# Kernel tuning notes

Hardware: AMD Instinct MI355X
Metric: run time of the kernel (lower is better)

The kernel has to match this reference:

```python
import jax, jax.numpy as jnp
import numpy as np

BETA = 0.25  # commit loss weight (init arg beta)


def setup_inputs() -> dict:
    key = jax.random.key(0)
    k1, k2 = jax.random.split(key)
    z = jax.random.normal(k1, (8, 8192, 128), dtype=jnp.float32)          # (B, T, D)
    codebook = jax.random.normal(k2, (1024, 128), dtype=jnp.float32)      # (K, D)
    return {"z": z, "codebook": codebook}


def reference(z, codebook):
    # distances: ||z - e||^2 = -2 z.e + ||z||^2 + ||e||^2
    dot = jnp.einsum('btd,kd->btk', z, codebook)                 # (B, T, K)
    norm_sq_z = jnp.sum(jnp.square(z), axis=-1, keepdims=True)   # (B, T, 1)
    norm_sq_e = jnp.sum(jnp.square(codebook), axis=-1)           # (K,)
    dist = -2.0 * dot + norm_sq_z + norm_sq_e                    # (B, T, K)
    ids = jnp.argmin(dist, axis=-1)                              # (B, T) int
    z_q = codebook[ids]                                          # gather -> (B, T, D)
    similarity = dot / jnp.sqrt(norm_sq_z) / jnp.sqrt(norm_sq_e) # cosine sim (B, T, K)
    # VQ loss (mean over batch*time of L2 norms along channel axis)
    loss_codebook = jnp.mean(jnp.linalg.norm(z - jax.lax.stop_gradient(z_q), axis=-1))
    loss_commit = jnp.mean(jnp.linalg.norm(jax.lax.stop_gradient(z) - z_q, axis=-1))
    loss_vq = loss_codebook + BETA * loss_commit
    return z_q, similarity, ids, loss_vq
```

## Files before the change

kernel.cpp:

```cpp
#include <hip/hip_runtime.h>
#include <hip/hip_bf16.h>


#define BT_TOTAL 65536
#define DDIM 128
#define KCODES 1024
#define ROWS 64
#define KC 64
#define NCHUNK (KCODES / KC)
#define TAU 0.125f


__global__ __launch_bounds__(256) void vq_pre_transpose(const float* __restrict__ e,
                                                        float* __restrict__ e_t) {
    int g = blockIdx.x * 256 + threadIdx.x;
    int d = g >> 10;
    int k = g & 1023;
    e_t[d * KCODES + k] = e[k * DDIM + d];
}

__global__ __launch_bounds__(256) void vq_pre_norms(const float* __restrict__ e,
                                                    float* __restrict__ ne,
                                                    float* __restrict__ ine) {
    int code = blockIdx.x * 4 + (threadIdx.x >> 6);
    int lane = threadIdx.x & 63;
    float v0 = e[code * DDIM + lane];
    float v1 = e[code * DDIM + lane + 64];
    float s = v0 * v0 + v1 * v1;
    #pragma unroll
    for (int m = 1; m < 64; m <<= 1) s += __shfl_xor(s, m);
    if (lane == 0) { ne[code] = s; ine[code] = rsqrtf(s); }
}


__global__ __launch_bounds__(256, 2) void vq_main(
    const float* __restrict__ z, const float* __restrict__ cb,
    const float* __restrict__ e_t, const float* __restrict__ ne_g,
    const float* __restrict__ ine_g,
    float* __restrict__ zq_out, float* __restrict__ sim_out,
    float* __restrict__ ids_out, float* __restrict__ loss_out,
    int* __restrict__ fix_cnt, int* __restrict__ fix_rows)
{
    __shared__ float lds_z[DDIM][ROWS];
    __shared__ float lds_e[DDIM][KC];
    __shared__ float lds_nzp[4][ROWS];
    __shared__ float lds_nz[ROWS];
    __shared__ float lds_inz[ROWS];
    __shared__ int   lds_best[ROWS];
    __shared__ float lds_loss[16];

    const int t = threadIdx.x;
    const int row_base = blockIdx.x * ROWS;

    #pragma unroll
    for (int it = 0; it < 8; ++it) {
        int idx = t + 256 * it;
        int row = idx & 63;
        int q   = idx >> 6;
        const float4 v = reinterpret_cast<const float4*>(z)[(size_t)(row_base + row) * 32 + q];
        lds_z[4 * q + 0][row] = v.x;
        lds_z[4 * q + 1][row] = v.y;
        lds_z[4 * q + 2][row] = v.z;
        lds_z[4 * q + 3][row] = v.w;
    }
    __syncthreads();

    {
        int row = t & 63, dp = t >> 6;
        float s = 0.f;
        #pragma unroll 8
        for (int d0 = 0; d0 < 32; ++d0) {
            float v = lds_z[dp * 32 + d0][row];
            s = fmaf(v, v, s);
        }
        lds_nzp[dp][row] = s;
    }
    __syncthreads();
    if (t < ROWS) {
        float s = lds_nzp[0][t] + lds_nzp[1][t] + lds_nzp[2][t] + lds_nzp[3][t];
        lds_nz[t]  = s;
        lds_inz[t] = rsqrtf(s);
    }
    __syncthreads();

    const int r = t >> 4;
    const int c = t & 15;

    float nzr[4], inzr[4];
    #pragma unroll
    for (int i = 0; i < 4; ++i) { nzr[i] = lds_nz[4 * r + i]; inzr[i] = lds_inz[4 * r + i]; }

    float runmin[4], runmin2[4]; int runidx[4];
    #pragma unroll
    for (int i = 0; i < 4; ++i) { runmin[i] = 3.4e38f; runmin2[i] = 3.4e38f; runidx[i] = 0; }

    for (int chunk = 0; chunk < NCHUNK; ++chunk) {
        const int kb = chunk * KC;

        #pragma unroll
        for (int j = 0; j < 8; ++j) {
            int idx = t + 256 * j;
            int d  = idx >> 4;
            int cc = idx & 15;
            float4 v = reinterpret_cast<const float4*>(e_t)[d * (KCODES / 4) + (kb >> 2) + cc];
            *reinterpret_cast<float4*>(&lds_e[d][4 * cc]) = v;
        }
        __syncthreads();

        float acc[4][4];
        #pragma unroll
        for (int i = 0; i < 4; ++i)
            #pragma unroll
            for (int j = 0; j < 4; ++j) acc[i][j] = 0.f;

        #pragma unroll 8
        for (int d = 0; d < DDIM; ++d) {
            float4 zv = *reinterpret_cast<const float4*>(&lds_z[d][4 * r]);
            float4 ev = *reinterpret_cast<const float4*>(&lds_e[d][4 * c]);
            float za[4] = { zv.x, zv.y, zv.z, zv.w };
            float ea[4] = { ev.x, ev.y, ev.z, ev.w };
            #pragma unroll
            for (int i = 0; i < 4; ++i)
                #pragma unroll
                for (int j = 0; j < 4; ++j)
                    acc[i][j] = fmaf(za[i], ea[j], acc[i][j]);
        }

        const float4 nev  = reinterpret_cast<const float4*>(ne_g)[chunk * 16 + c];
        const float4 inev = reinterpret_cast<const float4*>(ine_g)[chunk * 16 + c];
        float nea[4]  = { nev.x, nev.y, nev.z, nev.w };
        float inea[4] = { inev.x, inev.y, inev.z, inev.w };

        #pragma unroll
        for (int i = 0; i < 4; ++i) {
            float sa[4];
            #pragma unroll
            for (int j = 0; j < 4; ++j) {
                float dot = acc[i][j];
                sa[j] = dot * inzr[i] * inea[j];
                float dd = ((-2.0f * dot) + nzr[i]) + nea[j];
                int kidx = kb + 4 * c + j;
                if (dd < runmin[i]) { runmin2[i] = runmin[i]; runmin[i] = dd; runidx[i] = kidx; }
                else if (dd < runmin2[i]) runmin2[i] = dd;
            }
            float4 sv; sv.x = sa[0]; sv.y = sa[1]; sv.z = sa[2]; sv.w = sa[3];
            reinterpret_cast<float4*>(sim_out)[(size_t)(row_base + 4 * r + i) * (KCODES / 4) + (kb >> 2) + c] = sv;
        }
        __syncthreads();
    }

    #pragma unroll
    for (int m = 1; m < 16; m <<= 1) {
        #pragma unroll
        for (int i = 0; i < 4; ++i) {
            float om1 = __shfl_xor(runmin[i], m);
            float om2 = __shfl_xor(runmin2[i], m);
            int   oi  = __shfl_xor(runidx[i], m);
            float nm2 = fminf(fminf(runmin2[i], om2), fmaxf(runmin[i], om1));
            if (om1 < runmin[i] || (om1 == runmin[i] && oi < runidx[i])) {
                runmin[i] = om1; runidx[i] = oi;
            }
            runmin2[i] = nm2;
        }
    }
    if (c == 0) {
        float psum = 0.f;
        #pragma unroll
        for (int i = 0; i < 4; ++i) {
            int row = 4 * r + i;
            lds_best[row] = runidx[i];
            ids_out[row_base + row] = (float)runidx[i];
            psum += sqrtf(fmaxf(runmin[i], 0.f));
            if (runmin2[i] - runmin[i] < TAU) {
                int slot = atomicAdd(fix_cnt, 1);
                fix_rows[slot] = row_base + row;
            }
        }
        lds_loss[r] = psum;
    }
    __syncthreads();

    if (t == 0) {
        float s = 0.f;
        #pragma unroll
        for (int i = 0; i < 16; ++i) s += lds_loss[i];
        atomicAdd(loss_out, s * (1.25f / 65536.0f));
    }

    #pragma unroll
    for (int j2 = 0; j2 < 8; ++j2) {
        int idx = t + 256 * j2;
        int row = idx >> 5;
        int q   = idx & 31;
        int b   = lds_best[row];
        float4 v = reinterpret_cast<const float4*>(cb)[b * 32 + q];
        reinterpret_cast<float4*>(zq_out)[(size_t)(row_base + row) * 32 + q] = v;
    }
}


__global__ __launch_bounds__(256) void vq_fixup(
    const float* __restrict__ z, const float* __restrict__ cb,
    const float* __restrict__ e_t,
    const int* __restrict__ fix_cnt, const int* __restrict__ fix_rows,
    float* __restrict__ zq_out, float* __restrict__ ids_out)
{
    __shared__ float zl[DDIM];
    __shared__ double wbest[4];
    __shared__ int    wbidx[4];
    const int n = *fix_cnt;
    const int tid = threadIdx.x;

    for (int item = blockIdx.x; item < n; item += gridDim.x) {
        const int row = fix_rows[item];
        if (tid < DDIM) zl[tid] = z[(size_t)row * DDIM + tid];
        __syncthreads();

        double bd = 1.0e300; int bi = 0;
        #pragma unroll
        for (int c4 = 0; c4 < 4; ++c4) {
            const int code = c4 * 256 + tid;
            double acc = 0.0;
            #pragma unroll 4
            for (int d = 0; d < DDIM; ++d) {
                double diff = (double)zl[d] - (double)e_t[d * KCODES + code];
                acc = fma(diff, diff, acc);
            }
            if (acc < bd) { bd = acc; bi = code; }
        }
        const int lane = tid & 63, w = tid >> 6;
        #pragma unroll
        for (int m = 1; m < 64; m <<= 1) {
            double od = __shfl_xor(bd, m);
            int    oi = __shfl_xor(bi, m);
            if (od < bd || (od == bd && oi < bi)) { bd = od; bi = oi; }
        }
        if (lane == 0) { wbest[w] = bd; wbidx[w] = bi; }
        __syncthreads();
        if (tid == 0) {
            double b0 = wbest[0]; int i0 = wbidx[0];
            #pragma unroll
            for (int i = 1; i < 4; ++i)
                if (wbest[i] < b0 || (wbest[i] == b0 && wbidx[i] < i0)) { b0 = wbest[i]; i0 = wbidx[i]; }
            wbidx[0] = i0;
            ids_out[row] = (float)i0;
        }
        __syncthreads();
        const int b = wbidx[0];
        if (tid < 32) {
            float4 v = reinterpret_cast<const float4*>(cb)[b * 32 + tid];
            reinterpret_cast<float4*>(zq_out)[(size_t)row * 32 + tid] = v;
        }
        __syncthreads();
    }
}


extern "C" void kernel_launch(void* const* d_in, const int* in_sizes, int n_in,
                              void* d_out, int out_size, void* d_ws, size_t ws_size,
                              hipStream_t stream) {
    const float* z  = (const float*)d_in[0];
    const float* cb = (const float*)d_in[1];

    float* out  = (float*)d_out;
    float* zq   = out;
    float* sim  = out + 8388608;
    float* ids  = out + 75497472;
    float* loss = out + 75563008;

    float* e_t      = (float*)d_ws;
    float* ne       = e_t + 131072;
    float* ine      = ne + 1024;
    int*   fix_cnt  = (int*)(ine + 1024);
    int*   fix_rows = fix_cnt + 1;

    hipMemsetAsync(loss, 0, sizeof(float), stream);
    hipMemsetAsync(fix_cnt, 0, sizeof(int), stream);

    vq_pre_transpose<<<512, 256, 0, stream>>>(cb, e_t);
    vq_pre_norms<<<256, 256, 0, stream>>>(cb, ne, ine);
    vq_main<<<BT_TOTAL / ROWS, 256, 0, stream>>>(z, cb, e_t, ne, ine,
                                                 zq, sim, ids, loss, fix_cnt, fix_rows);
    vq_fixup<<<256, 256, 0, stream>>>(z, cb, e_t, fix_cnt, fix_rows, zq, ids);
}
```

Baseline: 690.8 us.

## Compute distance GEMM with split-bf16 MFMA instead of FP32 FMA

Replaces the LDS-tiled FP32 FMA dot-product loop with bf16 MFMA instructions, using a hi/lo bf16 split of both z and the codebook and three MFMAs to approximate FP32 precision. Each wave keeps its 32 rows of z in registers and streams codebook fragments directly from global memory without LDS staging. Row norms of z now come from a separate pre-pass kernel, and the codebook is pre-split into bf16 hi/lo arrays. The risks are reduced dot-product precision that the tau-based fixup has to absorb, and a similarity store pattern of scalar, strided writes that may coalesce worse than the earlier float4 stores.

```diff
diff --git a/kernel.cpp b/kernel.cpp
--- a/kernel.cpp
+++ b/kernel.cpp
@@ -5,18 +5,38 @@
 #define BT_TOTAL 65536
 #define DDIM 128
 #define KCODES 1024
-#define ROWS 64
-#define KC 64
-#define NCHUNK (KCODES / KC)
 #define TAU 0.125f
 
-
-__global__ __launch_bounds__(256) void vq_pre_transpose(const float* __restrict__ e,
-                                                        float* __restrict__ e_t) {
-    int g = blockIdx.x * 256 + threadIdx.x;
-    int d = g >> 10;
-    int k = g & 1023;
-    e_t[d * KCODES + k] = e[k * DDIM + d];
+typedef __attribute__((ext_vector_type(8))) short bf16x8;
+typedef __attribute__((ext_vector_type(4))) float f32x4;
+
+__device__ __forceinline__ unsigned short f32_to_bf16_rne(float x) {
+    unsigned int u = __float_as_uint(x);
+    unsigned int r = u + 0x7FFFu + ((u >> 16) & 1u);
+    return (unsigned short)(r >> 16);
+}
+__device__ __forceinline__ float bf16u_to_f32(unsigned short s) {
+    return __uint_as_float(((unsigned int)s) << 16);
+}
+
+
+__global__ __launch_bounds__(256) void vq_pre_cb(const float* __restrict__ cb,
+                                                 unsigned short* __restrict__ cb_hi,
+                                                 unsigned short* __restrict__ cb_lo) {
+    int gidx = blockIdx.x * 256 + threadIdx.x;
+    float4 v = reinterpret_cast<const float4*>(cb)[gidx];
+    float a[4] = { v.x, v.y, v.z, v.w };
+    ushort4 h, l;
+    unsigned short hs[4], ls[4];
+    #pragma unroll
+    for (int j = 0; j < 4; ++j) {
+        hs[j] = f32_to_bf16_rne(a[j]);
+        ls[j] = f32_to_bf16_rne(a[j] - bf16u_to_f32(hs[j]));
+    }
+    h.x = hs[0]; h.y = hs[1]; h.z = hs[2]; h.w = hs[3];
+    l.x = ls[0]; l.y = ls[1]; l.z = ls[2]; l.w = ls[3];
+    reinterpret_cast<ushort4*>(cb_hi)[gidx] = h;
+    reinterpret_cast<ushort4*>(cb_lo)[gidx] = l;
 }
 
 __global__ __launch_bounds__(256) void vq_pre_norms(const float* __restrict__ e,
@@ -32,169 +52,178 @@
     if (lane == 0) { ne[code] = s; ine[code] = rsqrtf(s); }
 }
 
+__global__ __launch_bounds__(256) void vq_pre_transpose(const float* __restrict__ e,
+                                                        float* __restrict__ e_t) {
+    int g = blockIdx.x * 256 + threadIdx.x;
+    int d = g >> 10;
+    int k = g & 1023;
+    e_t[d * KCODES + k] = e[k * DDIM + d];
+}
+
+__global__ __launch_bounds__(256) void vq_pre_znorm(const float* __restrict__ z,
+                                                    float* __restrict__ nz) {
+    int wg = blockIdx.x * 4 + (threadIdx.x >> 6);
+    int lane = threadIdx.x & 63;
+    #pragma unroll
+    for (int it = 0; it < 8; ++it) {
+        int row = wg + 8192 * it;
+        float2 v = reinterpret_cast<const float2*>(z)[(size_t)row * 64 + lane];
+        float s = v.x * v.x + v.y * v.y;
+        #pragma unroll
+        for (int m = 1; m < 64; m <<= 1) s += __shfl_xor(s, m);
+        if (lane == 0) nz[row] = s;
+    }
+}
+
 
 __global__ __launch_bounds__(256, 2) void vq_main(
     const float* __restrict__ z, const float* __restrict__ cb,
-    const float* __restrict__ e_t, const float* __restrict__ ne_g,
-    const float* __restrict__ ine_g,
+    const unsigned short* __restrict__ cb_hi, const unsigned short* __restrict__ cb_lo,
+    const float* __restrict__ ne_g, const float* __restrict__ ine_g,
+    const float* __restrict__ nz_g,
     float* __restrict__ zq_out, float* __restrict__ sim_out,
     float* __restrict__ ids_out, float* __restrict__ loss_out,
     int* __restrict__ fix_cnt, int* __restrict__ fix_rows)
 {
-    __shared__ float lds_z[DDIM][ROWS];
-    __shared__ float lds_e[DDIM][KC];
-    __shared__ float lds_nzp[4][ROWS];
-    __shared__ float lds_nz[ROWS];
-    __shared__ float lds_inz[ROWS];
-    __shared__ int   lds_best[ROWS];
-    __shared__ float lds_loss[16];
+    __shared__ int s_best[4][32];
 
     const int t = threadIdx.x;
-    const int row_base = blockIdx.x * ROWS;
-
-    #pragma unroll
-    for (int it = 0; it < 8; ++it) {
-        int idx = t + 256 * it;
-        int row = idx & 63;
-        int q   = idx >> 6;
-        const float4 v = reinterpret_cast<const float4*>(z)[(size_t)(row_base + row) * 32 + q];
-        lds_z[4 * q + 0][row] = v.x;
-        lds_z[4 * q + 1][row] = v.y;
-        lds_z[4 * q + 2][row] = v.z;
-        lds_z[4 * q + 3][row] = v.w;
-    }
+    const int wave = t >> 6, lane = t & 63;
+    const int g = lane >> 4, li = lane & 15;
+    const int rbase = (blockIdx.x * 4 + wave) * 32;
+
+    bf16x8 Ah[2][4], Al[2][4];
+    #pragma unroll
+    for (int rt = 0; rt < 2; ++rt) {
+        const int row = rbase + rt * 16 + li;
+        const float4* pz = reinterpret_cast<const float4*>(z + (size_t)row * DDIM);
+        #pragma unroll
+        for (int ks = 0; ks < 4; ++ks) {
+            float4 v0 = pz[ks * 8 + g * 2];
+            float4 v1 = pz[ks * 8 + g * 2 + 1];
+            float a[8] = { v0.x, v0.y, v0.z, v0.w, v1.x, v1.y, v1.z, v1.w };
+            bf16x8 h, lo;
+            #pragma unroll
+            for (int j = 0; j < 8; ++j) {
+                unsigned short hs = f32_to_bf16_rne(a[j]);
+                float fh = bf16u_to_f32(hs);
+                unsigned short ls = f32_to_bf16_rne(a[j] - fh);
+                h[j] = (short)hs; lo[j] = (short)ls;
+            }
+            Ah[rt][ks] = h; Al[rt][ks] = lo;
+        }
+    }
+
+    float nzr[2][4], inzr[2][4];
+    #pragma unroll
+    for (int rt = 0; rt < 2; ++rt)
+        #pragma unroll
+        for (int q = 0; q < 4; ++q) {
+            float n = nz_g[rbase + rt * 16 + g * 4 + q];
+            nzr[rt][q] = n; inzr[rt][q] = rsqrtf(n);
+        }
+
+    float runmin[2][4], runmin2[2][4]; int runidx[2][4];
+    #pragma unroll
+    for (int rt = 0; rt < 2; ++rt)
+        #pragma unroll
+        for (int q = 0; q < 4; ++q) { runmin[rt][q] = 3.4e38f; runmin2[rt][q] = 3.4e38f; runidx[rt][q] = 0; }
+
+    for (int chunk = 0; chunk < 32; ++chunk) {
+        const int cbase = chunk * 32;
+        f32x4 acc[2][2];
+        #pragma unroll
+        for (int rt = 0; rt < 2; ++rt)
+            #pragma unroll
+            for (int ct = 0; ct < 2; ++ct) acc[rt][ct] = (f32x4){0.f, 0.f, 0.f, 0.f};
+
+        #pragma unroll
+        for (int ct = 0; ct < 2; ++ct) {
+            const int code = cbase + ct * 16 + li;
+            const bf16x8* ph = reinterpret_cast<const bf16x8*>(cb_hi + (size_t)code * DDIM);
+            const bf16x8* pl = reinterpret_cast<const bf16x8*>(cb_lo + (size_t)code * DDIM);
+            bf16x8 Bh[4], Bl[4];
+            #pragma unroll
+            for (int ks = 0; ks < 4; ++ks) { Bh[ks] = ph[ks * 4 + g]; Bl[ks] = pl[ks * 4 + g]; }
+            #pragma unroll
+            for (int ks = 0; ks < 4; ++ks) {
+                #pragma unroll
+                for (int rt = 0; rt < 2; ++rt) {
+                    acc[rt][ct] = __builtin_amdgcn_mfma_f32_16x16x32_bf16(Ah[rt][ks], Bh[ks], acc[rt][ct], 0, 0, 0);
+                    acc[rt][ct] = __builtin_amdgcn_mfma_f32_16x16x32_bf16(Ah[rt][ks], Bl[ks], acc[rt][ct], 0, 0, 0);
+                    acc[rt][ct] = __builtin_amdgcn_mfma_f32_16x16x32_bf16(Al[rt][ks], Bh[ks], acc[rt][ct], 0, 0, 0);
+                }
+            }
+        }
+
+        #pragma unroll
+        for (int ct = 0; ct < 2; ++ct) {
+            const int code = cbase + ct * 16 + li;
+            const float ne_c = ne_g[code], ine_c = ine_g[code];
+            #pragma unroll
+            for (int rt = 0; rt < 2; ++rt) {
+                #pragma unroll
+                for (int q = 0; q < 4; ++q) {
+                    float dot = acc[rt][ct][q];
+                    int row = rbase + rt * 16 + g * 4 + q;
+                    sim_out[(size_t)row * KCODES + code] = dot * inzr[rt][q] * ine_c;
+                    float dd = ((-2.0f * dot) + nzr[rt][q]) + ne_c;
+                    if (dd < runmin[rt][q]) {
+                        runmin2[rt][q] = runmin[rt][q]; runmin[rt][q] = dd; runidx[rt][q] = code;
+                    } else if (dd < runmin2[rt][q]) runmin2[rt][q] = dd;
+                }
+            }
+        }
+    }
+
+    #pragma unroll
+    for (int m = 1; m < 16; m <<= 1) {
+        #pragma unroll
+        for (int rt = 0; rt < 2; ++rt)
+            #pragma unroll
+            for (int q = 0; q < 4; ++q) {
+                float om1 = __shfl_xor(runmin[rt][q], m);
+                float om2 = __shfl_xor(runmin2[rt][q], m);
+                int   oi  = __shfl_xor(runidx[rt][q], m);
+                float nm2 = fminf(fminf(runmin2[rt][q], om2), fmaxf(runmin[rt][q], om1));
+                if (om1 < runmin[rt][q] || (om1 == runmin[rt][q] && oi < runidx[rt][q])) {
+                    runmin[rt][q] = om1; runidx[rt][q] = oi;
+                }
+                runmin2[rt][q] = nm2;
+            }
+    }
+
+    float loss_p = 0.f;
+    if (li == 0) {
+        #pragma unroll
+        for (int rt = 0; rt < 2; ++rt)
+            #pragma unroll
+            for (int q = 0; q < 4; ++q) {
+                int rl = rt * 16 + g * 4 + q;
+                int idx = runidx[rt][q];
+                s_best[wave][rl] = idx;
+                ids_out[rbase + rl] = (float)idx;
+                loss_p += sqrtf(fmaxf(runmin[rt][q], 0.f));
+                if (runmin2[rt][q] - runmin[rt][q] < TAU) {
+                    int slot = atomicAdd(fix_cnt, 1);
+                    fix_rows[slot] = rbase + rl;
+                }
+            }
+    }
+    loss_p += __shfl_xor(loss_p, 16);
+    loss_p += __shfl_xor(loss_p, 32);
+    if (lane == 0) atomicAdd(loss_out, loss_p * (1.25f / 65536.0f));
+
     __syncthreads();
 
-    {
-        int row = t & 63, dp = t >> 6;
-        float s = 0.f;
-        #pragma unroll 8
-        for (int d0 = 0; d0 < 32; ++d0) {
-            float v = lds_z[dp * 32 + d0][row];
-            s = fmaf(v, v, s);
-        }
-        lds_nzp[dp][row] = s;
-    }
-    __syncthreads();
-    if (t < ROWS) {
-        float s = lds_nzp[0][t] + lds_nzp[1][t] + lds_nzp[2][t] + lds_nzp[3][t];
-        lds_nz[t]  = s;
-        lds_inz[t] = rsqrtf(s);
-    }
-    __syncthreads();
-
-    const int r = t >> 4;
-    const int c = t & 15;
-
-    float nzr[4], inzr[4];
-    #pragma unroll
-    for (int i = 0; i < 4; ++i) { nzr[i] = lds_nz[4 * r + i]; inzr[i] = lds_inz[4 * r + i]; }
-
-    float runmin[4], runmin2[4]; int runidx[4];
-    #pragma unroll
-    for (int i = 0; i < 4; ++i) { runmin[i] = 3.4e38f; runmin2[i] = 3.4e38f; runidx[i] = 0; }
-
-    for (int chunk = 0; chunk < NCHUNK; ++chunk) {
-        const int kb = chunk * KC;
-
-        #pragma unroll
-        for (int j = 0; j < 8; ++j) {
-            int idx = t + 256 * j;
-            int d  = idx >> 4;
-            int cc = idx & 15;
-            float4 v = reinterpret_cast<const float4*>(e_t)[d * (KCODES / 4) + (kb >> 2) + cc];
-            *reinterpret_cast<float4*>(&lds_e[d][4 * cc]) = v;
-        }
-        __syncthreads();
-
-        float acc[4][4];
-        #pragma unroll
-        for (int i = 0; i < 4; ++i)
-            #pragma unroll
-            for (int j = 0; j < 4; ++j) acc[i][j] = 0.f;
-
-        #pragma unroll 8
-        for (int d = 0; d < DDIM; ++d) {
-            float4 zv = *reinterpret_cast<const float4*>(&lds_z[d][4 * r]);
-            float4 ev = *reinterpret_cast<const float4*>(&lds_e[d][4 * c]);
-            float za[4] = { zv.x, zv.y, zv.z, zv.w };
-            float ea[4] = { ev.x, ev.y, ev.z, ev.w };
-            #pragma unroll
-            for (int i = 0; i < 4; ++i)
-                #pragma unroll
-                for (int j = 0; j < 4; ++j)
-                    acc[i][j] = fmaf(za[i], ea[j], acc[i][j]);
-        }
-
-        const float4 nev  = reinterpret_cast<const float4*>(ne_g)[chunk * 16 + c];
-        const float4 inev = reinterpret_cast<const float4*>(ine_g)[chunk * 16 + c];
-        float nea[4]  = { nev.x, nev.y, nev.z, nev.w };
-        float inea[4] = { inev.x, inev.y, inev.z, inev.w };
-
-        #pragma unroll
-        for (int i = 0; i < 4; ++i) {
-            float sa[4];
-            #pragma unroll
-            for (int j = 0; j < 4; ++j) {
-                float dot = acc[i][j];
-                sa[j] = dot * inzr[i] * inea[j];
-                float dd = ((-2.0f * dot) + nzr[i]) + nea[j];
-                int kidx = kb + 4 * c + j;
-                if (dd < runmin[i]) { runmin2[i] = runmin[i]; runmin[i] = dd; runidx[i] = kidx; }
-                else if (dd < runmin2[i]) runmin2[i] = dd;
-            }
-            float4 sv; sv.x = sa[0]; sv.y = sa[1]; sv.z = sa[2]; sv.w = sa[3];
-            reinterpret_cast<float4*>(sim_out)[(size_t)(row_base + 4 * r + i) * (KCODES / 4) + (kb >> 2) + c] = sv;
-        }
-        __syncthreads();
-    }
-
-    #pragma unroll
-    for (int m = 1; m < 16; m <<= 1) {
-        #pragma unroll
-        for (int i = 0; i < 4; ++i) {
-            float om1 = __shfl_xor(runmin[i], m);
-            float om2 = __shfl_xor(runmin2[i], m);
-            int   oi  = __shfl_xor(runidx[i], m);
-            float nm2 = fminf(fminf(runmin2[i], om2), fmaxf(runmin[i], om1));
-            if (om1 < runmin[i] || (om1 == runmin[i] && oi < runidx[i])) {
-                runmin[i] = om1; runidx[i] = oi;
-            }
-            runmin2[i] = nm2;
-        }
-    }
-    if (c == 0) {
-        float psum = 0.f;
-        #pragma unroll
-        for (int i = 0; i < 4; ++i) {
-            int row = 4 * r + i;
-            lds_best[row] = runidx[i];
-            ids_out[row_base + row] = (float)runidx[i];
-            psum += sqrtf(fmaxf(runmin[i], 0.f));
-            if (runmin2[i] - runmin[i] < TAU) {
-                int slot = atomicAdd(fix_cnt, 1);
-                fix_rows[slot] = row_base + row;
-            }
-        }
-        lds_loss[r] = psum;
-    }
-    __syncthreads();
-
-    if (t == 0) {
-        float s = 0.f;
-        #pragma unroll
-        for (int i = 0; i < 16; ++i) s += lds_loss[i];
-        atomicAdd(loss_out, s * (1.25f / 65536.0f));
-    }
-
-    #pragma unroll
-    for (int j2 = 0; j2 < 8; ++j2) {
-        int idx = t + 256 * j2;
-        int row = idx >> 5;
-        int q   = idx & 31;
-        int b   = lds_best[row];
-        float4 v = reinterpret_cast<const float4*>(cb)[b * 32 + q];
-        reinterpret_cast<float4*>(zq_out)[(size_t)(row_base + row) * 32 + q] = v;
+    #pragma unroll
+    for (int it = 0; it < 16; ++it) {
+        int idx2 = it * 64 + lane;
+        int rl = idx2 >> 5;
+        int qq = idx2 & 31;
+        int b = s_best[wave][rl];
+        float4 v = reinterpret_cast<const float4*>(cb)[b * 32 + qq];
+        reinterpret_cast<float4*>(zq_out)[(size_t)(rbase + rl) * 32 + qq] = v;
     }
 }
 
@@ -268,18 +297,24 @@
     float* ids  = out + 75497472;
     float* loss = out + 75563008;
 
-    float* e_t      = (float*)d_ws;
-    float* ne       = e_t + 131072;
-    float* ine      = ne + 1024;
-    int*   fix_cnt  = (int*)(ine + 1024);
-    int*   fix_rows = fix_cnt + 1;
+    float* e_t = (float*)d_ws;
+    float* ne  = e_t + 131072;
+    float* ine = ne + 1024;
+    float* nz  = ine + 1024;
+    unsigned short* cb_hi = (unsigned short*)(nz + 65536);
+    unsigned short* cb_lo = cb_hi + 131072;
+    int* fix_cnt  = (int*)(cb_lo + 131072);
+    int* fix_rows = fix_cnt + 1;
 
     hipMemsetAsync(loss, 0, sizeof(float), stream);
     hipMemsetAsync(fix_cnt, 0, sizeof(int), stream);
 
+    vq_pre_cb<<<128, 256, 0, stream>>>(cb, cb_hi, cb_lo);
+    vq_pre_norms<<<256, 256, 0, stream>>>(cb, ne, ine);
     vq_pre_transpose<<<512, 256, 0, stream>>>(cb, e_t);
-    vq_pre_norms<<<256, 256, 0, stream>>>(cb, ne, ine);
-    vq_main<<<BT_TOTAL / ROWS, 256, 0, stream>>>(z, cb, e_t, ne, ine,
-                                                 zq, sim, ids, loss, fix_cnt, fix_rows);
+    vq_pre_znorm<<<2048, 256, 0, stream>>>(z, nz);
+
+    vq_main<<<512, 256, 0, stream>>>(z, cb, cb_hi, cb_lo, ne, ine, nz,
+                                     zq, sim, ids, loss, fix_cnt, fix_rows);
     vq_fixup<<<256, 256, 0, stream>>>(z, cb, e_t, fix_cnt, fix_rows, zq, ids);
 }
```

Measured after the change: 634.7 us. -8.1%, faster.
